# Kernel tuning notes

Measured on AMD Instinct MI355X. Metric: run time of the kernel, lower is better.

## Reference

```python
import jax, jax.numpy as jnp
import numpy as np

IMAGE_SIZE = 256
SIGMA = 1.0   # soft-rasterization sharpness (pixels)
EPS = 1e-8


def _quat_to_rot(q):
    q = q / jnp.sqrt(jnp.sum(q * q) + EPS)
    w, x, y, z = q[0], q[1], q[2], q[3]
    return jnp.stack([
        jnp.stack([1 - 2 * (y * y + z * z), 2 * (x * y - w * z), 2 * (x * z + w * y)]),
        jnp.stack([2 * (x * y + w * z), 1 - 2 * (x * x + z * z), 2 * (y * z - w * x)]),
        jnp.stack([2 * (x * z - w * y), 2 * (y * z + w * x), 1 - 2 * (x * x + y * y)]),
    ])


def _render_silhouette(vertices, faces, q, t, K):
    # camera transform: v_cam = R(q) v + t   [V,3]
    R = _quat_to_rot(q)
    vc = vertices[0] @ R.T + t
    z = vc[:, 2] + EPS
    # perspective projection to pixel coords
    px_v = K[0, 0] * vc[:, 0] / z + K[0, 2]
    py_v = K[1, 1] * vc[:, 1] / z + K[1, 2]
    verts2d = jnp.stack([px_v, py_v], axis=-1)          # [V,2]
    tri = verts2d[faces[0]]                             # [F,3,2]

    e01 = tri[:, 1] - tri[:, 0]
    e02 = tri[:, 2] - tri[:, 0]
    area2 = e01[:, 0] * e02[:, 1] - e01[:, 1] * e02[:, 0]
    s = jnp.where(area2 >= 0, 1.0, -1.0)                # [F]

    # pixel centers
    ii, jj = jnp.meshgrid(jnp.arange(IMAGE_SIZE), jnp.arange(IMAGE_SIZE), indexing='ij')
    px = (jj.astype(jnp.float32) + 0.5).reshape(-1)     # [P]
    py = (ii.astype(jnp.float32) + 0.5).reshape(-1)     # [P]

    # signed distance to triangle = min over edges of normalized edge function
    d = None
    for k in range(3):
        a = tri[:, k]
        b = tri[:, (k + 1) % 3]
        ex = b[:, 0] - a[:, 0]
        ey = b[:, 1] - a[:, 1]
        inv_len = s / jnp.sqrt(ex * ex + ey * ey + EPS)  # sign folded in
        cx = -ey * inv_len
        cy = ex * inv_len
        c0 = (ey * a[:, 0] - ex * a[:, 1]) * inv_len
        c = px[:, None] * cx[None, :] + py[:, None] * cy[None, :] + c0[None, :]  # [P,F]
        d = c if d is None else jnp.minimum(d, c)

    # soft coverage: alpha = 1 - prod_F (1 - sigmoid(d/sigma))
    log_not_cov = jax.nn.log_sigmoid(-d / SIGMA)         # [P,F]
    sil = 1.0 - jnp.exp(jnp.sum(log_not_cov, axis=1))    # [P]
    return sil.reshape(IMAGE_SIZE, IMAGE_SIZE)


def setup_inputs() -> dict:
    key = jax.random.key(0)
    k1, k2, k3 = jax.random.split(key, 3)
    V, F = 1000, 1000
    vertices = jax.random.normal(k1, (1, V, 3), jnp.float32) * 0.3
    faces = jax.random.randint(k2, (1, F, 3), 0, V, jnp.int32)
    image_ref = jax.random.uniform(k3, (IMAGE_SIZE, IMAGE_SIZE), dtype=jnp.float32)
    q = jnp.array([1.0, 0.05, -0.03, 0.02], dtype=jnp.float32)
    t = jnp.array([0.0, 0.0, 2.732], dtype=jnp.float32)
    K = jnp.array([[280.0, 0.0, 128.0], [0.0, 280.0, 128.0], [0.0, 0.0, 1.0]], dtype=jnp.float32)
    return {"vertices": vertices, "faces": faces, "q": q, "t": t, "K": K, "image_ref": image_ref}


def reference(vertices, faces, q, t, K, image_ref):
    image = _render_silhouette(vertices, faces, q, t, K)   # [256,256]
    loss = jnp.mean((image - image_ref) ** 2, axis=1)      # per-row mean, [256]
    return loss
```

## Files before the change

### kernel.cpp

```cpp
#include <hip/hip_runtime.h>
#include <math.h>

#define IMG 256
#define NFACE 1000
#define NFP 1024
#define NWAVE 4
#define EPSF 1e-8f
#define LOG2E 1.44269504088896f
#define TCUT 16.0f
#define ACC_BREAK 25.0f
#define CULL_M (-(TCUT + 7.15f))

__device__ float g_soa[9][NFP];

__device__ __forceinline__ float bcast(float x, int s) {
    return __uint_as_float(__builtin_amdgcn_readlane(__float_as_uint(x), s));
}

__global__ __launch_bounds__(256) void k_coeff(const float* __restrict__ verts,
                                               const int* __restrict__ faces,
                                               const float* __restrict__ q,
                                               const float* __restrict__ t,
                                               const float* __restrict__ K,
                                               float* __restrict__ out) {
    int f = blockIdx.x * 256 + threadIdx.x;
    if (blockIdx.x == 0 && threadIdx.x < IMG) out[threadIdx.x] = 0.f;
    if (f >= NFP) return;

    float c[9];
    if (f < NFACE) {
        float qw = q[0], qx = q[1], qy = q[2], qz = q[3];
        float qn = sqrtf(qw * qw + qx * qx + qy * qy + qz * qz + EPSF);
        qw /= qn; qx /= qn; qy /= qn; qz /= qn;
        float R00 = 1.f - 2.f * (qy * qy + qz * qz);
        float R01 = 2.f * (qx * qy - qw * qz);
        float R02 = 2.f * (qx * qz + qw * qy);
        float R10 = 2.f * (qx * qy + qw * qz);
        float R11 = 1.f - 2.f * (qx * qx + qz * qz);
        float R12 = 2.f * (qy * qz - qw * qx);
        float R20 = 2.f * (qx * qz - qw * qy);
        float R21 = 2.f * (qy * qz + qw * qx);
        float R22 = 1.f - 2.f * (qx * qx + qy * qy);
        float tx = t[0], ty = t[1], tz = t[2];
        float K00 = K[0], K02 = K[2], K11 = K[4], K12 = K[5];

        float X[3], Y[3];
#pragma unroll
        for (int k = 0; k < 3; ++k) {
            int vi = faces[f * 3 + k];
            float vx = verts[vi * 3 + 0];
            float vy = verts[vi * 3 + 1];
            float vz = verts[vi * 3 + 2];
            float cx = R00 * vx + R01 * vy + R02 * vz + tx;
            float cy = R10 * vx + R11 * vy + R12 * vz + ty;
            float cz = R20 * vx + R21 * vy + R22 * vz + tz;
            float z = cz + EPSF;
            X[k] = K00 * cx / z + K02;
            Y[k] = K11 * cy / z + K12;
        }

        float e01x = X[1] - X[0], e01y = Y[1] - Y[0];
        float e02x = X[2] - X[0], e02y = Y[2] - Y[0];
        float area2 = e01x * e02y - e01y * e02x;
        float s = (area2 >= 0.f) ? LOG2E : -LOG2E;

#pragma unroll
        for (int k = 0; k < 3; ++k) {
            int k1 = (k + 1) % 3;
            float ex = X[k1] - X[k];
            float ey = Y[k1] - Y[k];
            float inv = s / sqrtf(ex * ex + ey * ey + EPSF);
            c[k * 3 + 0] = -ey * inv;
            c[k * 3 + 1] = ex * inv;
            c[k * 3 + 2] = (ey * X[k] - ex * Y[k]) * inv;
        }
    } else {
        c[0] = 0.f; c[1] = 0.f; c[2] = -1e9f;
        c[3] = 0.f; c[4] = 0.f; c[5] = -1e9f;
        c[6] = 0.f; c[7] = 0.f; c[8] = -1e9f;
    }

#pragma unroll
    for (int k = 0; k < 9; ++k) g_soa[k][f] = c[k];
}

__global__ __launch_bounds__(256) void k_main(const float* __restrict__ image_ref,
                                              float* __restrict__ out) {
    const int tid = threadIdx.x;
    const int wave = tid >> 6;
    const int lane = tid & 63;
    const int x0 = blockIdx.x * 8, y0 = blockIdx.y * 8;
    const int col = x0 + (lane & 7);
    const int row = y0 + (lane >> 3);
    const float px = col + 0.5f;
    const float py = row + 0.5f;
    const float tcx = x0 + 4.0f;
    const float tcy = y0 + 4.0f;

    __shared__ float s_acc[NWAVE][64];

    float acc = 0.f;
    const int wbase = wave * 256;
    for (int r = 0; r < 4; ++r) {
        const int f = wbase + r * 64 + lane;
        float l0 = g_soa[0][f], l1 = g_soa[1][f], l2 = g_soa[2][f];
        float l3 = g_soa[3][f], l4 = g_soa[4][f], l5 = g_soa[5][f];
        float l6 = g_soa[6][f], l7 = g_soa[7][f], l8 = g_soa[8][f];
        float m = fminf(fminf(fmaf(tcx, l0, fmaf(tcy, l1, l2)),
                              fmaf(tcx, l3, fmaf(tcy, l4, l5))),
                        fmaf(tcx, l6, fmaf(tcy, l7, l8)));
        unsigned long long msk = __ballot(m > CULL_M);
        float p = 1.f;
        while (msk) {
            int s = __ffsll((unsigned long long)msk) - 1;
            msk &= msk - 1;
            float a0 = bcast(l0, s), a1 = bcast(l1, s), a2 = bcast(l2, s);
            float b0 = bcast(l3, s), b1 = bcast(l4, s), b2 = bcast(l5, s);
            float c0 = bcast(l6, s), c1 = bcast(l7, s), c2 = bcast(l8, s);
            float u = fminf(fminf(fmaf(px, a0, fmaf(py, a1, a2)),
                                  fmaf(px, b0, fmaf(py, b1, b2))),
                            fmaf(px, c0, fmaf(py, c1, c2)));
            acc += fmaxf(u, 0.f);
            float e = __builtin_amdgcn_exp2f(-fabsf(u));
            p = fmaf(p, e, p);
        }
        acc += __builtin_amdgcn_logf(p);
        if (__all(acc > ACC_BREAK)) break;
    }

    s_acc[wave][lane] = acc;
    __syncthreads();
    if (wave == 0) {
        float tot = s_acc[0][lane] + s_acc[1][lane] +
                    s_acc[2][lane] + s_acc[3][lane];
        float sil = 1.f - __builtin_amdgcn_exp2f(-tot);
        float d = sil - image_ref[row * IMG + col];
        float v = d * d;
        v += __shfl_xor(v, 1);
        v += __shfl_xor(v, 2);
        v += __shfl_xor(v, 4);
        if ((lane & 7) == 0) atomicAdd(&out[row], v * (1.f / 256.f));
    }
}

extern "C" void kernel_launch(void* const* d_in, const int* in_sizes, int n_in,
                              void* d_out, int out_size, void* d_ws, size_t ws_size,
                              hipStream_t stream) {
    const float* verts = (const float*)d_in[0];
    const int* faces = (const int*)d_in[1];
    const float* q = (const float*)d_in[2];
    const float* t = (const float*)d_in[3];
    const float* K = (const float*)d_in[4];
    const float* image_ref = (const float*)d_in[5];
    float* out = (float*)d_out;

    k_coeff<<<NFP / 256, 256, 0, stream>>>(verts, faces, q, t, K, out);
    k_main<<<dim3(IMG / 8, IMG / 8), 256, 0, stream>>>(image_ref, out);
}
```

Measured before the change: 20.72 us.

## Pack four pixel tiles per 1024-thread block and unroll face loop by two

The main kernel now launches 256 blocks of 1024 threads. Each block handles four 8x8 tiles with four waves per tile, instead of one tile per 256-thread block, which reduces block count and scheduling overhead. The inner loop over surviving faces now processes two faces per iteration, with a guard weight for the odd leftover, to add instruction-level parallelism across the readlane broadcasts and exp2 calls. The risks are tighter register limits from the 1024-thread launch bound and extra wasted work when only one face remains in an iteration.

```diff
diff --git a/kernel.cpp b/kernel.cpp
--- a/kernel.cpp
+++ b/kernel.cpp
@@ -4,7 +4,6 @@
 #define IMG 256
 #define NFACE 1000
 #define NFP 1024
-#define NWAVE 4
 #define EPSF 1e-8f
 #define LOG2E 1.44269504088896f
 #define TCUT 16.0f
@@ -84,12 +83,15 @@
     for (int k = 0; k < 9; ++k) g_soa[k][f] = c[k];
 }
 
-__global__ __launch_bounds__(256) void k_main(const float* __restrict__ image_ref,
-                                              float* __restrict__ out) {
+__global__ __launch_bounds__(1024, 2) void k_main(const float* __restrict__ image_ref,
+                                                  float* __restrict__ out) {
     const int tid = threadIdx.x;
     const int wave = tid >> 6;
     const int lane = tid & 63;
-    const int x0 = blockIdx.x * 8, y0 = blockIdx.y * 8;
+    const int tlocal = wave >> 2;
+    const int wgrp = wave & 3;
+    const int tile = blockIdx.x + (tlocal << 8);
+    const int x0 = (tile & 31) * 8, y0 = (tile >> 5) * 8;
     const int col = x0 + (lane & 7);
     const int row = y0 + (lane >> 3);
     const float px = col + 0.5f;
@@ -97,10 +99,10 @@
     const float tcx = x0 + 4.0f;
     const float tcy = y0 + 4.0f;
 
-    __shared__ float s_acc[NWAVE][64];
+    __shared__ float s_acc[16][64];
 
     float acc = 0.f;
-    const int wbase = wave * 256;
+    const int wbase = wgrp * 256;
     for (int r = 0; r < 4; ++r) {
         const int f = wbase + r * 64 + lane;
         float l0 = g_soa[0][f], l1 = g_soa[1][f], l2 = g_soa[2][f];
@@ -112,17 +114,32 @@
         unsigned long long msk = __ballot(m > CULL_M);
         float p = 1.f;
         while (msk) {
-            int s = __ffsll((unsigned long long)msk) - 1;
+            int s0 = __ffsll((unsigned long long)msk) - 1;
             msk &= msk - 1;
-            float a0 = bcast(l0, s), a1 = bcast(l1, s), a2 = bcast(l2, s);
-            float b0 = bcast(l3, s), b1 = bcast(l4, s), b2 = bcast(l5, s);
-            float c0 = bcast(l6, s), c1 = bcast(l7, s), c2 = bcast(l8, s);
-            float u = fminf(fminf(fmaf(px, a0, fmaf(py, a1, a2)),
-                                  fmaf(px, b0, fmaf(py, b1, b2))),
-                            fmaf(px, c0, fmaf(py, c1, c2)));
-            acc += fmaxf(u, 0.f);
-            float e = __builtin_amdgcn_exp2f(-fabsf(u));
-            p = fmaf(p, e, p);
+            bool has1 = (msk != 0);
+            int s1 = has1 ? (__ffsll((unsigned long long)msk) - 1) : s0;
+            msk &= msk - 1;
+            float g1 = has1 ? 1.f : 0.f;
+
+            float a0 = bcast(l0, s0), a1 = bcast(l1, s0), a2 = bcast(l2, s0);
+            float b0 = bcast(l3, s0), b1 = bcast(l4, s0), b2 = bcast(l5, s0);
+            float c0 = bcast(l6, s0), c1 = bcast(l7, s0), c2 = bcast(l8, s0);
+            float A0 = bcast(l0, s1), A1 = bcast(l1, s1), A2 = bcast(l2, s1);
+            float B0 = bcast(l3, s1), B1 = bcast(l4, s1), B2 = bcast(l5, s1);
+            float C0 = bcast(l6, s1), C1 = bcast(l7, s1), C2 = bcast(l8, s1);
+
+            float u0 = fminf(fminf(fmaf(px, a0, fmaf(py, a1, a2)),
+                                   fmaf(px, b0, fmaf(py, b1, b2))),
+                             fmaf(px, c0, fmaf(py, c1, c2)));
+            float u1 = fminf(fminf(fmaf(px, A0, fmaf(py, A1, A2)),
+                                   fmaf(px, B0, fmaf(py, B1, B2))),
+                             fmaf(px, C0, fmaf(py, C1, C2)));
+
+            acc += fmaxf(u0, 0.f) + fmaxf(u1, 0.f) * g1;
+            float e0 = __builtin_amdgcn_exp2f(-fabsf(u0));
+            float e1 = __builtin_amdgcn_exp2f(-fabsf(u1)) * g1;
+            p = fmaf(p, e0, p);
+            p = fmaf(p, e1, p);
         }
         acc += __builtin_amdgcn_logf(p);
         if (__all(acc > ACC_BREAK)) break;
@@ -130,9 +147,9 @@
 
     s_acc[wave][lane] = acc;
     __syncthreads();
-    if (wave == 0) {
-        float tot = s_acc[0][lane] + s_acc[1][lane] +
-                    s_acc[2][lane] + s_acc[3][lane];
+    if (wgrp == 0) {
+        float tot = s_acc[wave][lane] + s_acc[wave + 1][lane] +
+                    s_acc[wave + 2][lane] + s_acc[wave + 3][lane];
         float sil = 1.f - __builtin_amdgcn_exp2f(-tot);
         float d = sil - image_ref[row * IMG + col];
         float v = d * d;
@@ -155,5 +172,5 @@
     float* out = (float*)d_out;
 
     k_coeff<<<NFP / 256, 256, 0, stream>>>(verts, faces, q, t, K, out);
-    k_main<<<dim3(IMG / 8, IMG / 8), 256, 0, stream>>>(image_ref, out);
+    k_main<<<256, 1024, 0, stream>>>(image_ref, out);
 }
```

Result: slower. 24.00 us (+15.8%).

## Add tile-level coverage bound to skip saturated tiles and tighten face culling

Applied to the files above, without the earlier changes.

Loads all four face groups' coefficients up front, then computes a tile-wide lower bound on the log-coverage sum (reduced across waves via shared memory). If that bound exceeds the saturation threshold, the tile skips per-pixel evaluation entirely. Otherwise the per-face cull test uses a per-edge tile-extent bound instead of a single slack constant, and an early-exit check runs every 8 faces inside the inner loop. The aim is to cut wasted work in saturated interior tiles. In exchange it adds a block-wide barrier, higher register pressure from holding 36 coefficients per lane, and a fixed accumulator value of 8 for saturated tiles that relies on the output being saturated.

```diff
diff --git a/kernel.cpp b/kernel.cpp
--- a/kernel.cpp
+++ b/kernel.cpp
@@ -9,7 +9,7 @@
 #define LOG2E 1.44269504088896f
 #define TCUT 16.0f
 #define ACC_BREAK 25.0f
-#define CULL_M (-(TCUT + 7.15f))
+#define RSLACK 7.15f
 
 __device__ float g_soa[9][NFP];
 
@@ -98,34 +98,77 @@
     const float tcy = y0 + 4.0f;
 
     __shared__ float s_acc[NWAVE][64];
-
-    float acc = 0.f;
+    __shared__ float s_S[NWAVE];
+
     const int wbase = wave * 256;
+
+    float l[4][9];
+#pragma unroll
     for (int r = 0; r < 4; ++r) {
         const int f = wbase + r * 64 + lane;
-        float l0 = g_soa[0][f], l1 = g_soa[1][f], l2 = g_soa[2][f];
-        float l3 = g_soa[3][f], l4 = g_soa[4][f], l5 = g_soa[5][f];
-        float l6 = g_soa[6][f], l7 = g_soa[7][f], l8 = g_soa[8][f];
-        float m = fminf(fminf(fmaf(tcx, l0, fmaf(tcy, l1, l2)),
-                              fmaf(tcx, l3, fmaf(tcy, l4, l5))),
-                        fmaf(tcx, l6, fmaf(tcy, l7, l8)));
-        unsigned long long msk = __ballot(m > CULL_M);
-        float p = 1.f;
-        while (msk) {
-            int s = __ffsll((unsigned long long)msk) - 1;
-            msk &= msk - 1;
-            float a0 = bcast(l0, s), a1 = bcast(l1, s), a2 = bcast(l2, s);
-            float b0 = bcast(l3, s), b1 = bcast(l4, s), b2 = bcast(l5, s);
-            float c0 = bcast(l6, s), c1 = bcast(l7, s), c2 = bcast(l8, s);
-            float u = fminf(fminf(fmaf(px, a0, fmaf(py, a1, a2)),
-                                  fmaf(px, b0, fmaf(py, b1, b2))),
-                            fmaf(px, c0, fmaf(py, c1, c2)));
-            acc += fmaxf(u, 0.f);
-            float e = __builtin_amdgcn_exp2f(-fabsf(u));
-            p = fmaf(p, e, p);
+#pragma unroll
+        for (int k = 0; k < 9; ++k) l[r][k] = g_soa[k][f];
+    }
+
+    unsigned long long msk0 = 0, msk1 = 0, msk2 = 0, msk3 = 0;
+    float slb = 0.f;
+#pragma unroll
+    for (int r = 0; r < 4; ++r) {
+        float c0 = fmaf(tcx, l[r][0], fmaf(tcy, l[r][1], l[r][2]));
+        float c1 = fmaf(tcx, l[r][3], fmaf(tcy, l[r][4], l[r][5]));
+        float c2 = fmaf(tcx, l[r][6], fmaf(tcy, l[r][7], l[r][8]));
+        float mc = fminf(fminf(c0, c1), c2);
+        slb += fmaxf(mc - RSLACK, 0.f);
+        float e0 = c0 + 3.5f * (fabsf(l[r][0]) + fabsf(l[r][1]));
+        float e1 = c1 + 3.5f * (fabsf(l[r][3]) + fabsf(l[r][4]));
+        float e2 = c2 + 3.5f * (fabsf(l[r][6]) + fabsf(l[r][7]));
+        float mx = fminf(fminf(e0, e1), e2);
+        unsigned long long mm = __ballot(mx > -TCUT);
+        if (r == 0) msk0 = mm;
+        else if (r == 1) msk1 = mm;
+        else if (r == 2) msk2 = mm;
+        else msk3 = mm;
+    }
+#pragma unroll
+    for (int o = 1; o < 64; o <<= 1) slb += __shfl_xor(slb, o);
+    if (lane == 0) s_S[wave] = slb;
+    __syncthreads();
+    const float S_tile = s_S[0] + s_S[1] + s_S[2] + s_S[3];
+
+    float acc;
+    if (S_tile > ACC_BREAK) {
+        acc = 8.f;
+    } else {
+        acc = 0.f;
+        int cnt = 0;
+        bool done = false;
+#pragma unroll
+        for (int r = 0; r < 4; ++r) {
+            if (!done) {
+                unsigned long long msk = (r == 0) ? msk0 : (r == 1) ? msk1
+                                       : (r == 2) ? msk2 : msk3;
+                float p = 1.f;
+                while (msk) {
+                    int s = __ffsll((unsigned long long)msk) - 1;
+                    msk &= msk - 1;
+                    float a0 = bcast(l[r][0], s), a1 = bcast(l[r][1], s), a2 = bcast(l[r][2], s);
+                    float b0 = bcast(l[r][3], s), b1 = bcast(l[r][4], s), b2 = bcast(l[r][5], s);
+                    float c0 = bcast(l[r][6], s), c1 = bcast(l[r][7], s), c2 = bcast(l[r][8], s);
+                    float u = fminf(fminf(fmaf(px, a0, fmaf(py, a1, a2)),
+                                          fmaf(px, b0, fmaf(py, b1, b2))),
+                                    fmaf(px, c0, fmaf(py, c1, c2)));
+                    acc += fmaxf(u, 0.f);
+                    float e = __builtin_amdgcn_exp2f(-fabsf(u));
+                    p = fmaf(p, e, p);
+                    if (((++cnt) & 7) == 0 && __all(acc > ACC_BREAK)) {
+                        done = true;
+                        break;
+                    }
+                }
+                acc += __builtin_amdgcn_logf(p);
+                if (__all(acc > ACC_BREAK)) done = true;
+            }
         }
-        acc += __builtin_amdgcn_logf(p);
-        if (__all(acc > ACC_BREAK)) break;
     }
 
     s_acc[wave][lane] = acc;
```

Result: no change. 20.83 us (+0.5%).
